# Kernel optimization log

Measured on AMD Instinct MI355X. Metric: run time of the kernel, lower is better.

## Reference

```python
import jax, jax.numpy as jnp
import numpy as np

B, H, W, C = 8, 64, 64, 256
RC = C // 8  # reduced channels per build()

def setup_inputs() -> dict:
    key = jax.random.key(0)
    ks = jax.random.split(key, 4)
    x = jax.random.normal(ks[0], (B, H, W, C), dtype=jnp.float32)
    # 1x1 conv kernels flattened to [Cin, Cout]; glorot-ish scale
    wq = jax.random.normal(ks[1], (C, RC), dtype=jnp.float32) * (1.0 / np.sqrt(C))
    wk = jax.random.normal(ks[2], (C, RC), dtype=jnp.float32) * (1.0 / np.sqrt(C))
    wv = jax.random.normal(ks[3], (C, C), dtype=jnp.float32) * (1.0 / np.sqrt(C))
    bq = jnp.zeros((RC,), dtype=jnp.float32)
    bk = jnp.zeros((RC,), dtype=jnp.float32)
    bv = jnp.zeros((C,), dtype=jnp.float32)
    return {"x": x, "wq": wq, "bq": bq, "wk": wk, "bk": bk, "wv": wv, "bv": bv}

def reference(x, wq, bq, wk, bk, wv, bv):
    b, h, w, c = x.shape
    n = h * w
    # 1x1 convs == per-pixel channel matmuls; q/k have relu activation, v does not
    q = jax.nn.relu(jnp.einsum('bhwc,cd->bhwd', x, wq) + bq).reshape(b, n, -1)  # [B,N,RC]
    k = jax.nn.relu(jnp.einsum('bhwc,cd->bhwd', x, wk) + bk).reshape(b, n, -1)  # [B,N,RC]
    v = (jnp.einsum('bhwc,cd->bhwd', x, wv) + bv).reshape(b, n, c)              # [B,N,C]
    attn = jax.nn.softmax(jnp.einsum('bnd,bmd->bnm', q, k), axis=-1)            # [B,N,N]
    out = jnp.einsum('bnm,bmc->bnc', attn, v).reshape(b, h, w, c)
    return out + x
```

## Files before the change

kernel.cpp:

```cpp
#include <hip/hip_runtime.h>
#include <hip/hip_bf16.h>

typedef __attribute__((ext_vector_type(8))) short s16x8;
typedef __attribute__((ext_vector_type(4))) float f32x4;
typedef __attribute__((ext_vector_type(4))) unsigned int u32x4;

#define BATCH 8
#define NPIX  4096
#define CCH   256
#define RCH   32
#define KVT   64
#define NT    (NPIX / KVT)
#define THR   8.0f
#define LOG2E 1.4426950408889634f

__device__ __forceinline__ unsigned short f2bf(float f) {
  __hip_bfloat16 h = __float2bfloat16(f);
  return __builtin_bit_cast(unsigned short, h);
}

__device__ __forceinline__ unsigned int pack_bf16(float lo, float hi) {
  return (unsigned int)f2bf(lo) | ((unsigned int)f2bf(hi) << 16);
}

__device__ __forceinline__ void gload_lds16(const void* g, void* l) {
  __builtin_amdgcn_global_load_lds(
      (const __attribute__((address_space(1))) void*)g,
      (__attribute__((address_space(3))) void*)l, 16, 0, 0);
}

__global__ void prep_kernel(const float* __restrict__ x,
                            const float* __restrict__ wq,
                            const float* __restrict__ wk,
                            const float* __restrict__ wv,
                            unsigned short* __restrict__ xb,
                            unsigned short* __restrict__ wqkT,
                            unsigned short* __restrict__ wvT) {
  int stride = gridDim.x * blockDim.x;
  int i0 = blockIdx.x * blockDim.x + threadIdx.x;
  const int nx4 = BATCH * NPIX * CCH / 4;
  for (int i = i0; i < nx4; i += stride) {
    float4 v = reinterpret_cast<const float4*>(x)[i];
    ushort4 o;
    o.x = f2bf(v.x); o.y = f2bf(v.y); o.z = f2bf(v.z); o.w = f2bf(v.w);
    reinterpret_cast<ushort4*>(xb)[i] = o;
  }
  for (int i = i0; i < 64 * CCH; i += stride) {
    int d = i >> 8, c = i & 255;
    float v = (d < RCH) ? wq[c * RCH + d] : wk[c * RCH + (d - RCH)];
    wqkT[i] = f2bf(v);
  }
  for (int i = i0; i < CCH * CCH; i += stride) {
    int d = i >> 8, c = i & 255;
    wvT[i] = f2bf(wv[c * CCH + d]);
  }
}

__global__ void qk_proj_kernel(const unsigned short* __restrict__ xb,
                               const unsigned short* __restrict__ wqkT,
                               const float* __restrict__ bq,
                               const float* __restrict__ bk,
                               unsigned short* __restrict__ qb,
                               unsigned short* __restrict__ kb) {
  int t = threadIdx.x;
  int w = t >> 6, l = t & 63, g = l >> 4, lc = l & 15;
  int row0 = blockIdx.x * 64 + w * 16;
  f32x4 zero = {0.f, 0.f, 0.f, 0.f};
  f32x4 acc[4];
  for (int ct = 0; ct < 4; ++ct) acc[ct] = zero;
  for (int ks = 0; ks < 8; ++ks) {
    s16x8 a = *reinterpret_cast<const s16x8*>(
        xb + (size_t)(row0 + lc) * CCH + ks * 32 + g * 8);
    for (int ct = 0; ct < 4; ++ct) {
      s16x8 bfr = *reinterpret_cast<const s16x8*>(
          wqkT + (size_t)(ct * 16 + lc) * CCH + ks * 32 + g * 8);
      acc[ct] = __builtin_amdgcn_mfma_f32_16x16x32_bf16(a, bfr, acc[ct], 0, 0, 0);
    }
  }
  for (int ct = 0; ct < 4; ++ct) {
    int col = ct * 16 + lc;
    float bias = (col < RCH) ? bq[col] : bk[col - RCH];
    for (int r = 0; r < 4; ++r) {
      int row = row0 + 4 * g + r;
      float v = fmaxf(acc[ct][r] + bias, 0.f);
      if (col < RCH) qb[(size_t)row * RCH + col] = f2bf(v * LOG2E);
      else           kb[(size_t)row * RCH + (col - RCH)] = f2bf(v);
    }
  }
}

__global__ void v_proj_kernel(const unsigned short* __restrict__ xb,
                              const unsigned short* __restrict__ wvT,
                              const float* __restrict__ bv,
                              unsigned short* __restrict__ vT) {
  int t = threadIdx.x;
  int w = t >> 6, l = t & 63, g = l >> 4, lc = l & 15;
  int idx = blockIdx.x;
  int b = idx & 7; idx >>= 3;
  int dt = idx & 3; int nt = idx >> 2;
  int d0 = dt * 64 + w * 16;
  int n0 = nt * 64;
  f32x4 zero = {0.f, 0.f, 0.f, 0.f};
  f32x4 acc[4];
  for (int ct = 0; ct < 4; ++ct) acc[ct] = zero;
  for (int ks = 0; ks < 8; ++ks) {
    s16x8 a = *reinterpret_cast<const s16x8*>(
        wvT + (size_t)(d0 + lc) * CCH + ks * 32 + g * 8);
    for (int ct = 0; ct < 4; ++ct) {
      s16x8 bfr = *reinterpret_cast<const s16x8*>(
          xb + ((size_t)b * NPIX + n0 + ct * 16 + lc) * CCH + ks * 32 + g * 8);
      acc[ct] = __builtin_amdgcn_mfma_f32_16x16x32_bf16(a, bfr, acc[ct], 0, 0, 0);
    }
  }
  for (int ct = 0; ct < 4; ++ct) {
    for (int r = 0; r < 4; ++r) {
      int d = d0 + 4 * g + r;
      int n = n0 + ct * 16 + lc;
      vT[((size_t)b * CCH + d) * NPIX + n] = f2bf(acc[ct][r] + bv[d]);
    }
  }
}

__global__ __launch_bounds__(256, 2)
void attn_kernel(const unsigned short* __restrict__ qb,
                 const unsigned short* __restrict__ kb,
                 const unsigned short* __restrict__ vT,
                 const float* __restrict__ x,
                 float* __restrict__ out) {
  __shared__ __attribute__((aligned(16))) unsigned short Vlds[2][CCH * KVT];
  __shared__ float lsumLds[64];

  int b  = blockIdx.x & 7;
  int qt = blockIdx.x >> 3;
  int t  = threadIdx.x;
  int w = t >> 6, l = t & 63, g = l >> 4, lc = l & 15;
  const size_t bN = (size_t)b * NPIX;
  f32x4 zero = {0.f, 0.f, 0.f, 0.f};

  const unsigned short* kbase = kb + bN * RCH;
  const unsigned short* vbase = vT + (size_t)b * CCH * NPIX;

  int qrow = qt * 64 + w * 16 + lc;
  s16x8 qfrag = *reinterpret_cast<const s16x8*>(qb + (bN + qrow) * RCH + g * 8);

  int chb = t >> 3, gr = t & 7;
  const unsigned short* vsrc =
      vbase + (size_t)chb * NPIX + ((gr ^ (chb & 7)) * 8);

  int krb = 8 * (lc >> 2) + (lc & 3);
  const int cto[4] = {0, 4, 32, 36};

  unsigned int swz = (lc & 7) << 4;
  int vr0 = (g * 16) ^ swz;
  int vr1 = (64 + g * 16) ^ swz;

  f32x4 o[16];
  #pragma unroll
  for (int cc = 0; cc < 16; ++cc) o[cc] = zero;
  float m = -1e30f, lsum = 0.f;

  #pragma unroll
  for (int i = 0; i < 8; ++i)
    gload_lds16(vsrc + (size_t)i * 32 * NPIX,
                (char*)&Vlds[0][0] + i * 4096 + t * 16);
  s16x8 kf[4];
  #pragma unroll
  for (int ct = 0; ct < 4; ++ct)
    kf[ct] = *reinterpret_cast<const s16x8*>(
        kbase + (size_t)(cto[ct] + krb) * RCH + g * 8);
  __syncthreads();

  for (int tix = 0; tix < NT; ++tix) {
    int p = tix & 1;
    int kv0 = tix * KVT;
    bool nx = (tix + 1) < NT;

    if (nx) {
      #pragma unroll
      for (int i = 0; i < 8; ++i)
        gload_lds16(vsrc + kv0 + KVT + (size_t)i * 32 * NPIX,
                    (char*)&Vlds[p ^ 1][0] + i * 4096 + t * 16);
    }

    f32x4 s[4];
    #pragma unroll
    for (int ct = 0; ct < 4; ++ct)
      s[ct] = __builtin_amdgcn_mfma_f32_16x16x32_bf16(kf[ct], qfrag, zero, 0, 0, 0);

    if (nx) {
      #pragma unroll
      for (int ct = 0; ct < 4; ++ct)
        kf[ct] = *reinterpret_cast<const s16x8*>(
            kbase + (size_t)(kv0 + KVT + cto[ct] + krb) * RCH + g * 8);
    }

    float pmax = s[0][0];
    #pragma unroll
    for (int ct = 0; ct < 4; ++ct)
      #pragma unroll
      for (int r = 0; r < 4; ++r) pmax = fmaxf(pmax, s[ct][r]);

    float sc = 1.f;
    int resc = !__all(pmax - m <= THR);
    if (resc) {
      #pragma unroll
      for (int off = 1; off <= 32; off <<= 1)
        pmax = fmaxf(pmax, __shfl_xor(pmax, off));
      float mnew = fmaxf(m, pmax);
      sc = exp2f(m - mnew);
      m = mnew;
    }

    float psum = 0.f;
    unsigned int pk[4][2];
    #pragma unroll
    for (int ct = 0; ct < 4; ++ct) {
      float p0 = exp2f(s[ct][0] - m);
      float p1 = exp2f(s[ct][1] - m);
      float p2 = exp2f(s[ct][2] - m);
      float p3 = exp2f(s[ct][3] - m);
      psum += (p0 + p1) + (p2 + p3);
      pk[ct][0] = pack_bf16(p0, p1);
      pk[ct][1] = pack_bf16(p2, p3);
    }
    lsum = lsum * sc + psum;

    if (resc) {
      #pragma unroll
      for (int cc = 0; cc < 16; ++cc)
        #pragma unroll
        for (int r = 0; r < 4; ++r) o[cc][r] *= sc;
    }

    u32x4 a0u = {pk[0][0], pk[0][1], pk[1][0], pk[1][1]};
    u32x4 a1u = {pk[2][0], pk[2][1], pk[3][0], pk[3][1]};
    s16x8 pa0 = __builtin_bit_cast(s16x8, a0u);
    s16x8 pa1 = __builtin_bit_cast(s16x8, a1u);
    const char* pb = (const char*)&Vlds[p][0] + lc * 128;
    __builtin_amdgcn_s_setprio(1);
    #pragma unroll
    for (int cc = 0; cc < 16; ++cc) {
      s16x8 vb0 = *reinterpret_cast<const s16x8*>(pb + cc * 2048 + vr0);
      s16x8 vb1 = *reinterpret_cast<const s16x8*>(pb + cc * 2048 + vr1);
      o[cc] = __builtin_amdgcn_mfma_f32_16x16x32_bf16(pa0, vb0, o[cc], 0, 0, 0);
      o[cc] = __builtin_amdgcn_mfma_f32_16x16x32_bf16(pa1, vb1, o[cc], 0, 0, 0);
    }
    __builtin_amdgcn_s_setprio(0);

    __syncthreads();
  }

  lsum += __shfl_xor(lsum, 16);
  lsum += __shfl_xor(lsum, 32);
  if (l < 16) lsumLds[w * 16 + l] = lsum;
  __syncthreads();

  f32x4 l4 = *reinterpret_cast<const f32x4*>(&lsumLds[w * 16 + 4 * g]);
  f32x4 rl;
  #pragma unroll
  for (int r = 0; r < 4; ++r) rl[r] = 1.0f / l4[r];

  #pragma unroll
  for (int cc = 0; cc < 16; ++cc) {
    #pragma unroll
    for (int r = 0; r < 4; ++r) {
      size_t row = bN + qt * 64 + w * 16 + 4 * g + r;
      size_t idx = row * CCH + cc * 16 + lc;
      out[idx] = o[cc][r] * rl[r] + x[idx];
    }
  }
}

extern "C" void kernel_launch(void* const* d_in, const int* in_sizes, int n_in,
                              void* d_out, int out_size, void* d_ws, size_t ws_size,
                              hipStream_t stream) {
  const float* x  = (const float*)d_in[0];
  const float* wq = (const float*)d_in[1];
  const float* bq = (const float*)d_in[2];
  const float* wk = (const float*)d_in[3];
  const float* bk = (const float*)d_in[4];
  const float* wv = (const float*)d_in[5];
  const float* bv = (const float*)d_in[6];
  float* out = (float*)d_out;

  unsigned short* ws   = (unsigned short*)d_ws;
  unsigned short* qb   = ws;
  unsigned short* kb   = qb + 1048576;
  unsigned short* vT   = kb + 1048576;
  unsigned short* xb   = vT + 8388608;
  unsigned short* wqkT = xb + 8388608;
  unsigned short* wvT  = wqkT + 16384;

  prep_kernel<<<dim3(2048), dim3(256), 0, stream>>>(x, wq, wk, wv, xb, wqkT, wvT);
  qk_proj_kernel<<<dim3(512), dim3(256), 0, stream>>>(xb, wqkT, bq, bk, qb, kb);
  v_proj_kernel<<<dim3(2048), dim3(256), 0, stream>>>(xb, wvT, bv, vT);
  attn_kernel<<<dim3(512), dim3(256), 0, stream>>>(qb, kb, vT, x, out);
}
```

Before: 166.7 us.

## Split KV sequence across wave pairs with 32-row query tiles per wave

Each wave now handles 32 query rows, two 16-row halves, over half of the key/value sequence, rather than 16 rows over all keys. Each V fragment read from LDS now feeds two MFMAs, which halves LDS read traffic per MFMA. The two halves of the sequence are merged at the end through LDS using each pair's running max and row sums. In exchange the accumulator register footprint doubles (o[2][16]) and there is an extra merge phase. The max is shared between the two query halves, which may cost some exp precision or cause more rescales.

```diff
diff --git a/kernel.cpp b/kernel.cpp
--- a/kernel.cpp
+++ b/kernel.cpp
@@ -9,8 +9,9 @@
 #define NPIX  4096
 #define CCH   256
 #define RCH   32
-#define KVT   64
-#define NT    (NPIX / KVT)
+#define TK    32
+#define HALFK 2048
+#define NIT   (HALFK / TK)
 #define THR   8.0f
 #define LOG2E 1.4426950408889634f
 
@@ -127,79 +128,81 @@
                  const unsigned short* __restrict__ vT,
                  const float* __restrict__ x,
                  float* __restrict__ out) {
-  __shared__ __attribute__((aligned(16))) unsigned short Vlds[2][CCH * KVT];
-  __shared__ float lsumLds[64];
+  __shared__ __attribute__((aligned(16))) unsigned short Vlds[2][CCH * 64];
+  __shared__ __attribute__((aligned(16))) float lsumLds[2][2][32];
+  __shared__ float mLds[2];
 
   int b  = blockIdx.x & 7;
   int qt = blockIdx.x >> 3;
   int t  = threadIdx.x;
   int w = t >> 6, l = t & 63, g = l >> 4, lc = l & 15;
+  int a = w >> 1, s = w & 1;
   const size_t bN = (size_t)b * NPIX;
   f32x4 zero = {0.f, 0.f, 0.f, 0.f};
 
   const unsigned short* kbase = kb + bN * RCH;
   const unsigned short* vbase = vT + (size_t)b * CCH * NPIX;
 
-  int qrow = qt * 64 + w * 16 + lc;
-  s16x8 qfrag = *reinterpret_cast<const s16x8*>(qb + (bN + qrow) * RCH + g * 8);
+  int qbase = qt * 64 + a * 32;
+  s16x8 qfA = *reinterpret_cast<const s16x8*>(qb + (bN + qbase + lc) * RCH + g * 8);
+  s16x8 qfB = *reinterpret_cast<const s16x8*>(qb + (bN + qbase + 16 + lc) * RCH + g * 8);
 
   int chb = t >> 3, gr = t & 7;
-  const unsigned short* vsrc =
-      vbase + (size_t)chb * NPIX + ((gr ^ (chb & 7)) * 8);
+  int gsw = gr ^ (chb & 7);
+  int koff = (gsw < 4) ? (gsw * 8) : (HALFK + (gsw - 4) * 8);
+  const unsigned short* vsrc = vbase + (size_t)chb * NPIX + koff;
 
   int krb = 8 * (lc >> 2) + (lc & 3);
-  const int cto[4] = {0, 4, 32, 36};
+  int kO  = s * HALFK + krb;
 
   unsigned int swz = (lc & 7) << 4;
-  int vr0 = (g * 16) ^ swz;
-  int vr1 = (64 + g * 16) ^ swz;
-
-  f32x4 o[16];
+  int vrS = (s * 64 + g * 16) ^ swz;
+
+  f32x4 o[2][16];
   #pragma unroll
-  for (int cc = 0; cc < 16; ++cc) o[cc] = zero;
-  float m = -1e30f, lsum = 0.f;
+  for (int qh = 0; qh < 2; ++qh)
+    #pragma unroll
+    for (int cc = 0; cc < 16; ++cc) o[qh][cc] = zero;
+  float m = -1e30f, lsum0 = 0.f, lsum1 = 0.f;
 
   #pragma unroll
   for (int i = 0; i < 8; ++i)
     gload_lds16(vsrc + (size_t)i * 32 * NPIX,
                 (char*)&Vlds[0][0] + i * 4096 + t * 16);
-  s16x8 kf[4];
-  #pragma unroll
-  for (int ct = 0; ct < 4; ++ct)
-    kf[ct] = *reinterpret_cast<const s16x8*>(
-        kbase + (size_t)(cto[ct] + krb) * RCH + g * 8);
+  s16x8 kf0 = *reinterpret_cast<const s16x8*>(kbase + (size_t)(kO + 0) * RCH + g * 8);
+  s16x8 kf1 = *reinterpret_cast<const s16x8*>(kbase + (size_t)(kO + 4) * RCH + g * 8);
   __syncthreads();
 
-  for (int tix = 0; tix < NT; ++tix) {
-    int p = tix & 1;
-    int kv0 = tix * KVT;
-    bool nx = (tix + 1) < NT;
+  for (int it = 0; it < NIT; ++it) {
+    int p = it & 1;
+    int kv = it * TK;
+    bool nx = (it + 1) < NIT;
 
     if (nx) {
       #pragma unroll
       for (int i = 0; i < 8; ++i)
-        gload_lds16(vsrc + kv0 + KVT + (size_t)i * 32 * NPIX,
+        gload_lds16(vsrc + kv + TK + (size_t)i * 32 * NPIX,
                     (char*)&Vlds[p ^ 1][0] + i * 4096 + t * 16);
     }
 
-    f32x4 s[4];
-    #pragma unroll
-    for (int ct = 0; ct < 4; ++ct)
-      s[ct] = __builtin_amdgcn_mfma_f32_16x16x32_bf16(kf[ct], qfrag, zero, 0, 0, 0);
+    f32x4 sA0 = __builtin_amdgcn_mfma_f32_16x16x32_bf16(kf0, qfA, zero, 0, 0, 0);
+    f32x4 sA1 = __builtin_amdgcn_mfma_f32_16x16x32_bf16(kf1, qfA, zero, 0, 0, 0);
+    f32x4 sB0 = __builtin_amdgcn_mfma_f32_16x16x32_bf16(kf0, qfB, zero, 0, 0, 0);
+    f32x4 sB1 = __builtin_amdgcn_mfma_f32_16x16x32_bf16(kf1, qfB, zero, 0, 0, 0);
 
     if (nx) {
-      #pragma unroll
-      for (int ct = 0; ct < 4; ++ct)
-        kf[ct] = *reinterpret_cast<const s16x8*>(
-            kbase + (size_t)(kv0 + KVT + cto[ct] + krb) * RCH + g * 8);
-    }
-
-    float pmax = s[0][0];
-    #pragma unroll
-    for (int ct = 0; ct < 4; ++ct)
-      #pragma unroll
-      for (int r = 0; r < 4; ++r) pmax = fmaxf(pmax, s[ct][r]);
-
+      kf0 = *reinterpret_cast<const s16x8*>(
+          kbase + (size_t)(kO + kv + TK + 0) * RCH + g * 8);
+      kf1 = *reinterpret_cast<const s16x8*>(
+          kbase + (size_t)(kO + kv + TK + 4) * RCH + g * 8);
+    }
+
+    float pmax = sA0[0];
+    #pragma unroll
+    for (int r = 0; r < 4; ++r) {
+      pmax = fmaxf(pmax, sA0[r]); pmax = fmaxf(pmax, sA1[r]);
+      pmax = fmaxf(pmax, sB0[r]); pmax = fmaxf(pmax, sB1[r]);
+    }
     float sc = 1.f;
     int resc = !__all(pmax - m <= THR);
     if (resc) {
@@ -211,62 +214,99 @@
       m = mnew;
     }
 
-    float psum = 0.f;
-    unsigned int pk[4][2];
-    #pragma unroll
-    for (int ct = 0; ct < 4; ++ct) {
-      float p0 = exp2f(s[ct][0] - m);
-      float p1 = exp2f(s[ct][1] - m);
-      float p2 = exp2f(s[ct][2] - m);
-      float p3 = exp2f(s[ct][3] - m);
-      psum += (p0 + p1) + (p2 + p3);
-      pk[ct][0] = pack_bf16(p0, p1);
-      pk[ct][1] = pack_bf16(p2, p3);
-    }
-    lsum = lsum * sc + psum;
+    float psA = 0.f, psB = 0.f;
+    unsigned int pkA[4], pkB[4];
+    {
+      float e0 = exp2f(sA0[0] - m), e1 = exp2f(sA0[1] - m);
+      float e2 = exp2f(sA0[2] - m), e3 = exp2f(sA0[3] - m);
+      psA += (e0 + e1) + (e2 + e3);
+      pkA[0] = pack_bf16(e0, e1); pkA[1] = pack_bf16(e2, e3);
+      e0 = exp2f(sA1[0] - m); e1 = exp2f(sA1[1] - m);
+      e2 = exp2f(sA1[2] - m); e3 = exp2f(sA1[3] - m);
+      psA += (e0 + e1) + (e2 + e3);
+      pkA[2] = pack_bf16(e0, e1); pkA[3] = pack_bf16(e2, e3);
+      e0 = exp2f(sB0[0] - m); e1 = exp2f(sB0[1] - m);
+      e2 = exp2f(sB0[2] - m); e3 = exp2f(sB0[3] - m);
+      psB += (e0 + e1) + (e2 + e3);
+      pkB[0] = pack_bf16(e0, e1); pkB[1] = pack_bf16(e2, e3);
+      e0 = exp2f(sB1[0] - m); e1 = exp2f(sB1[1] - m);
+      e2 = exp2f(sB1[2] - m); e3 = exp2f(sB1[3] - m);
+      psB += (e0 + e1) + (e2 + e3);
+      pkB[2] = pack_bf16(e0, e1); pkB[3] = pack_bf16(e2, e3);
+    }
+    lsum0 = lsum0 * sc + psA;
+    lsum1 = lsum1 * sc + psB;
 
     if (resc) {
       #pragma unroll
-      for (int cc = 0; cc < 16; ++cc)
+      for (int qh = 0; qh < 2; ++qh)
         #pragma unroll
-        for (int r = 0; r < 4; ++r) o[cc][r] *= sc;
-    }
-
-    u32x4 a0u = {pk[0][0], pk[0][1], pk[1][0], pk[1][1]};
-    u32x4 a1u = {pk[2][0], pk[2][1], pk[3][0], pk[3][1]};
-    s16x8 pa0 = __builtin_bit_cast(s16x8, a0u);
-    s16x8 pa1 = __builtin_bit_cast(s16x8, a1u);
-    const char* pb = (const char*)&Vlds[p][0] + lc * 128;
+        for (int cc = 0; cc < 16; ++cc)
+          #pragma unroll
+          for (int r = 0; r < 4; ++r) o[qh][cc][r] *= sc;
+    }
+
+    u32x4 uA = {pkA[0], pkA[1], pkA[2], pkA[3]};
+    u32x4 uB = {pkB[0], pkB[1], pkB[2], pkB[3]};
+    s16x8 paA = __builtin_bit_cast(s16x8, uA);
+    s16x8 paB = __builtin_bit_cast(s16x8, uB);
+    const char* pb = (const char*)&Vlds[p][0] + lc * 128 + vrS;
     __builtin_amdgcn_s_setprio(1);
     #pragma unroll
     for (int cc = 0; cc < 16; ++cc) {
-      s16x8 vb0 = *reinterpret_cast<const s16x8*>(pb + cc * 2048 + vr0);
-      s16x8 vb1 = *reinterpret_cast<const s16x8*>(pb + cc * 2048 + vr1);
-      o[cc] = __builtin_amdgcn_mfma_f32_16x16x32_bf16(pa0, vb0, o[cc], 0, 0, 0);
-      o[cc] = __builtin_amdgcn_mfma_f32_16x16x32_bf16(pa1, vb1, o[cc], 0, 0, 0);
+      s16x8 vb = *reinterpret_cast<const s16x8*>(pb + cc * 2048);
+      o[0][cc] = __builtin_amdgcn_mfma_f32_16x16x32_bf16(paA, vb, o[0][cc], 0, 0, 0);
+      o[1][cc] = __builtin_amdgcn_mfma_f32_16x16x32_bf16(paB, vb, o[1][cc], 0, 0, 0);
     }
     __builtin_amdgcn_s_setprio(0);
 
     __syncthreads();
   }
 
-  lsum += __shfl_xor(lsum, 16);
-  lsum += __shfl_xor(lsum, 32);
-  if (l < 16) lsumLds[w * 16 + l] = lsum;
+  lsum0 += __shfl_xor(lsum0, 16); lsum0 += __shfl_xor(lsum0, 32);
+  lsum1 += __shfl_xor(lsum1, 16); lsum1 += __shfl_xor(lsum1, 32);
+  if (l < 16) {
+    lsumLds[s][a][l]      = lsum0;
+    lsumLds[s][a][16 + l] = lsum1;
+  }
+  if (s == 1 && l == 0) mLds[a] = m;
   __syncthreads();
 
-  f32x4 l4 = *reinterpret_cast<const f32x4*>(&lsumLds[w * 16 + 4 * g]);
-  f32x4 rl;
-  #pragma unroll
-  for (int r = 0; r < 4; ++r) rl[r] = 1.0f / l4[r];
-
-  #pragma unroll
-  for (int cc = 0; cc < 16; ++cc) {
-    #pragma unroll
-    for (int r = 0; r < 4; ++r) {
-      size_t row = bN + qt * 64 + w * 16 + 4 * g + r;
-      size_t idx = row * CCH + cc * 16 + lc;
-      out[idx] = o[cc][r] * rl[r] + x[idx];
+  float* mrg = (float*)&Vlds[0][0];
+  if (s == 1) {
+    float* base = mrg + a * 8192 + l * 128;
+    #pragma unroll
+    for (int qh = 0; qh < 2; ++qh)
+      #pragma unroll
+      for (int cc = 0; cc < 16; ++cc) {
+        int idx = qh * 16 + cc;
+        *reinterpret_cast<f32x4*>(base + ((idx + l) & 31) * 4) = o[qh][cc];
+      }
+  }
+  __syncthreads();
+  if (s == 0) {
+    float mB = mLds[a];
+    float mT = fmaxf(m, mB);
+    float sAc = exp2f(m - mT), sBc = exp2f(mB - mT);
+    const float* base = mrg + a * 8192 + l * 128;
+    #pragma unroll
+    for (int qh = 0; qh < 2; ++qh) {
+      f32x4 lA4 = *reinterpret_cast<const f32x4*>(&lsumLds[0][a][qh * 16 + 4 * g]);
+      f32x4 lB4 = *reinterpret_cast<const f32x4*>(&lsumLds[1][a][qh * 16 + 4 * g]);
+      f32x4 rl;
+      #pragma unroll
+      for (int r = 0; r < 4; ++r) rl[r] = 1.0f / (lA4[r] * sAc + lB4[r] * sBc);
+      #pragma unroll
+      for (int cc = 0; cc < 16; ++cc) {
+        int idx = qh * 16 + cc;
+        f32x4 ob = *reinterpret_cast<const f32x4*>(base + ((idx + l) & 31) * 4);
+        #pragma unroll
+        for (int r = 0; r < 4; ++r) {
+          size_t row = bN + qbase + qh * 16 + 4 * g + r;
+          size_t oi = row * CCH + cc * 16 + lc;
+          out[oi] = (o[qh][cc][r] * sAc + ob[r] * sBc) * rl[r] + x[oi];
+        }
+      }
     }
   }
 }
```

After: 168.0 us. Within noise of the previous version (+0.8%).
